# Kernel tuning notes

Measured on AMD Instinct MI355X. Metric: run time of the kernel, lower is better.

The kernel has to match this reference:

```python
import jax, jax.numpy as jnp
import numpy as np

DIM = 512
NUM_HEAD = 8
HEAD_DIM = DIM // NUM_HEAD
FFN = 4 * DIM


def setup_inputs() -> dict:
    key = jax.random.key(0)
    ks = jax.random.split(key, 16)
    s = DIM ** -0.5
    inp = {
        "x": jax.random.normal(ks[0], (4, 2048, DIM), jnp.float32),
        "wq": jax.random.normal(ks[1], (DIM, DIM), jnp.float32) * s,
        "bq": jnp.zeros((DIM,), jnp.float32),
        "wk": jax.random.normal(ks[2], (DIM, DIM), jnp.float32) * s,
        "bk": jnp.zeros((DIM,), jnp.float32),
        "wv": jax.random.normal(ks[3], (DIM, DIM), jnp.float32) * s,
        "bv": jnp.zeros((DIM,), jnp.float32),
        "wo": jax.random.normal(ks[4], (DIM, DIM), jnp.float32) * s,
        "bo": jnp.zeros((DIM,), jnp.float32),
        "w1": jax.random.normal(ks[5], (DIM, FFN), jnp.float32) * s,
        "b1": jnp.zeros((FFN,), jnp.float32),
        "w2": jax.random.normal(ks[6], (FFN, DIM), jnp.float32) * (FFN ** -0.5),
        "b2": jnp.zeros((DIM,), jnp.float32),
        "g1": jnp.ones((DIM,), jnp.float32),
        "be1": jnp.zeros((DIM,), jnp.float32),
        "g2": jnp.ones((DIM,), jnp.float32),
        "be2": jnp.zeros((DIM,), jnp.float32),
    }
    return inp


def layer_norm(x, g, b, eps=1e-5):
    mu = jnp.mean(x, axis=-1, keepdims=True)
    var = jnp.var(x, axis=-1, keepdims=True)
    return (x - mu) * jax.lax.rsqrt(var + eps) * g + b


def _forward(x, wq, bq, wk, bk, wv, bv, wo, bo, w1, b1, w2, b2, g1, be1, g2, be2):
    b, n, _ = x.shape
    scale = HEAD_DIM ** -0.5
    q = (x @ wq + bq).reshape(b, n, NUM_HEAD, HEAD_DIM).transpose(0, 2, 1, 3)
    k = (x @ wk + bk).reshape(b, n, NUM_HEAD, HEAD_DIM).transpose(0, 2, 1, 3)
    v = (x @ wv + bv).reshape(b, n, NUM_HEAD, HEAD_DIM).transpose(0, 2, 1, 3)
    scores = jnp.einsum('bhqd,bhkd->bhqk', q, k) * scale
    attn = jax.nn.softmax(scores, axis=-1)
    out = jnp.einsum('bhqk,bhkd->bhqd', attn, v)
    out = out.transpose(0, 2, 1, 3).reshape(b, n, DIM)
    out = out @ wo + bo
    x = layer_norm(out + x, g1, be1)
    h = jax.nn.gelu(x @ w1 + b1, approximate=False)
    ff = h @ w2 + b2
    x = layer_norm(ff + x, g2, be2)
    return x


def reference(x, wq, bq, wk, bk, wv, bv, wo, bo, w1, b1, w2, b2, g1, be1, g2, be2):
    return _forward(x, wq, bq, wk, bk, wv, bv, wo, bo, w1, b1, w2, b2, g1, be1, g2, be2)
```

## Files before the change

### kernel.cpp

```cpp
#include <hip/hip_runtime.h>
#include <math.h>

#define DIM 512
#define NHEAD 8
#define HD 64
#define FFN_DIM 2048
#define BATCH 4
#define SEQ 2048
#define MTOK (BATCH*SEQ)

typedef __attribute__((ext_vector_type(8))) short bf16x8;
typedef __attribute__((ext_vector_type(4))) float f32x4;

__device__ __forceinline__ unsigned short f2b(float f){
    unsigned int u = __float_as_uint(f);
    u += 0x7fffu + ((u >> 16) & 1u);
    return (unsigned short)(u >> 16);
}
__device__ __forceinline__ float b2f(unsigned short u){
    return __uint_as_float(((unsigned int)u) << 16);
}
__device__ __forceinline__ unsigned int pack_trunc(float f0, float f1){
    return __builtin_amdgcn_perm(__float_as_uint(f1), __float_as_uint(f0), 0x07060302u);
}
__device__ __forceinline__ void async_cp16(const unsigned short* g, unsigned short* l){
    __builtin_amdgcn_global_load_lds((const __attribute__((address_space(1))) unsigned int*)g,
                                     (__attribute__((address_space(3))) unsigned int*)l, 16, 0, 0);
}
__device__ __forceinline__ float gelu_fast(float x){
    float x3 = x*x*x;
    float y  = 2.302588f * (x + 0.044715f*x3);
    float t  = __builtin_amdgcn_exp2f(y);
    return x * t * __builtin_amdgcn_rcpf(t + 1.0f);
}

__device__ __forceinline__ void transp32(const float* __restrict__ in, unsigned short* __restrict__ out,
                                         int N, int K, int n0_rd, int n0_wr, int k0,
                                         unsigned short (&t)[32][33], int tid){
    int tx = tid & 31, ty = tid >> 5;
    #pragma unroll
    for (int u = 0; u < 4; u++)
        t[tx][ty + 8*u] = f2b(in[(size_t)(k0 + ty + 8*u)*N + n0_rd + tx]);
    __syncthreads();
    #pragma unroll
    for (int u = 0; u < 4; u++)
        out[(size_t)(n0_wr + ty + 8*u)*K + k0 + tx] = t[ty + 8*u][tx];
}

__global__ void prep_kernel(const float* __restrict__ x,
                            const float* __restrict__ wq, const float* __restrict__ wk,
                            const float* __restrict__ wv, const float* __restrict__ wo,
                            const float* __restrict__ w1, const float* __restrict__ w2,
                            const float* __restrict__ bq, const float* __restrict__ bk,
                            const float* __restrict__ bv,
                            unsigned short* __restrict__ xb, unsigned short* __restrict__ wqkvT,
                            unsigned short* __restrict__ woT, unsigned short* __restrict__ w1T,
                            unsigned short* __restrict__ w2T, float* __restrict__ bqkv)
{
    __shared__ unsigned short t[32][33];
    int bid = blockIdx.x, tid = threadIdx.x;
    if (bid < 4096) {
        int i = (bid*256 + tid)*4;
        float4 v = *(const float4*)(x + i);
        ushort4 o; o.x=f2b(v.x); o.y=f2b(v.y); o.z=f2b(v.z); o.w=f2b(v.w);
        *(ushort4*)(xb + i) = o;
    } else if (bid < 4864) {
        int r = bid - 4096;
        int n0 = (r % 48)*32, k0 = (r / 48)*32;
        const float* w = (n0 < 512) ? wq : (n0 < 1024) ? wk : wv;
        transp32(w, wqkvT, 512, 512, n0 & 511, n0, k0, t, tid);
    } else if (bid < 5120) {
        int r = bid - 4864;
        int n0 = (r % 16)*32, k0 = (r / 16)*32;
        transp32(wo, woT, 512, 512, n0, n0, k0, t, tid);
    } else if (bid < 6144) {
        int r = bid - 5120;
        int n0 = (r % 64)*32, k0 = (r / 64)*32;
        transp32(w1, w1T, 2048, 512, n0, n0, k0, t, tid);
    } else if (bid < 7168) {
        int r = bid - 6144;
        int n0 = (r % 16)*32, k0 = (r / 16)*32;
        transp32(w2, w2T, 512, 2048, n0, n0, k0, t, tid);
    } else {
        int i = (bid - 7168)*256 + tid;
        if (i < 1536)
            bqkv[i] = (i < 512) ? bq[i] : (i < 1024) ? bk[i-512] : bv[i-1024];
    }
}

template<int MODE, int SK>
__global__ __launch_bounds__(256, 4)
void gemm_bf16(const unsigned short* __restrict__ A, const unsigned short* __restrict__ Bt,
               const float* __restrict__ bias,
               unsigned short* __restrict__ Cb,
               unsigned short* __restrict__ qo, unsigned short* __restrict__ ko,
               unsigned short* __restrict__ vTo,
               int M, int N, int K)
{
    __shared__ unsigned short As[128*64];
    __shared__ unsigned short Bs[128*64];
    int tid  = threadIdx.x;
    int lane = tid & 63;
    int ln = lane & 15, qd = lane >> 4;
    int m0 = blockIdx.x * 128, n0 = blockIdx.y * 128;
    int wid = tid >> 6;
    int wm = (wid >> 1) * 64;
    int wn = (wid & 1) * 64;
    int kbeg = (SK > 1) ? (int)blockIdx.z * (K/SK) : 0;
    int kend = kbeg + K/SK;
    if (SK > 1 && MODE == 0) Cb += (size_t)blockIdx.z * M * N;

    f32x4 acc[4][4];
    #pragma unroll
    for (int i = 0; i < 4; i++)
        #pragma unroll
        for (int j = 0; j < 4; j++) acc[i][j] = (f32x4){0.f,0.f,0.f,0.f};

    for (int k0 = kbeg; k0 < kend; k0 += 64) {
        #pragma unroll
        for (int i = 0; i < 4; i++) {
            int cid = i*256 + tid;
            int row = cid >> 3, cs = cid & 7;
            int cg = cs ^ (row & 7);
            async_cp16(&A[(size_t)(m0+row)*K + k0 + cg*8], &As[(cid & ~63) * 8]);
        }
        #pragma unroll
        for (int i = 0; i < 4; i++) {
            int cid = i*256 + tid;
            int row = cid >> 3, cs = cid & 7;
            int cg = cs ^ (row & 7);
            async_cp16(&Bt[(size_t)(n0+row)*K + k0 + cg*8], &Bs[(cid & ~63) * 8]);
        }
        __syncthreads();
        #pragma unroll
        for (int kk = 0; kk < 64; kk += 32) {
            int c0 = kk >> 3;
            bf16x8 af[4], bf[4];
            #pragma unroll
            for (int t = 0; t < 4; t++)
                af[t] = *(bf16x8*)&As[(wm + t*16 + ln)*64 + ((c0 + qd) ^ (ln & 7))*8];
            #pragma unroll
            for (int t = 0; t < 4; t++)
                bf[t] = *(bf16x8*)&Bs[(wn + t*16 + ln)*64 + ((c0 + qd) ^ (ln & 7))*8];
            #pragma unroll
            for (int i = 0; i < 4; i++)
                #pragma unroll
                for (int j = 0; j < 4; j++)
                    acc[i][j] = __builtin_amdgcn_mfma_f32_16x16x32_bf16(af[i], bf[j], acc[i][j], 0,0,0);
        }
        __syncthreads();
    }

    const float QSCALE = 0.18033688011112042f;
    #pragma unroll
    for (int i = 0; i < 4; i++) {
        int mb = m0 + wm + i*16 + qd*4;
        #pragma unroll
        for (int j = 0; j < 4; j++) {
            int c = n0 + wn + j*16 + ln;
            float bv_ = (SK > 1 && blockIdx.z) ? 0.f : bias[c];
            float v[4];
            #pragma unroll
            for (int r = 0; r < 4; r++) v[r] = acc[i][j][r] + bv_;
            if (MODE == 0) {
                #pragma unroll
                for (int r = 0; r < 4; r++) Cb[(size_t)(mb+r)*N + c] = f2b(v[r]);
            } else if (MODE == 2) {
                #pragma unroll
                for (int r = 0; r < 4; r++)
                    Cb[(size_t)(mb+r)*N + c] = f2b(gelu_fast(v[r]));
            } else {
                int b = mb >> 11, t0 = mb & 2047;
                if (c < 512) {
                    int h = c >> 6, hd = c & 63;
                    #pragma unroll
                    for (int r = 0; r < 4; r++)
                        qo[(((size_t)(b*8 + h))*SEQ + t0 + r)*64 + hd] = f2b(v[r] * QSCALE);
                } else if (c < 1024) {
                    int cc = c - 512, h = cc >> 6, hd = cc & 63;
                    #pragma unroll
                    for (int r = 0; r < 4; r++)
                        ko[(((size_t)(b*8 + h))*SEQ + t0 + r)*64 + hd] = f2b(v[r]);
                } else {
                    int cc = c - 1024, h = cc >> 6, hd = cc & 63;
                    ushort4 pk;
                    pk.x = f2b(v[0]); pk.y = f2b(v[1]); pk.z = f2b(v[2]); pk.w = f2b(v[3]);
                    *(ushort4*)&vTo[(((size_t)(b*8 + h))*64 + hd)*SEQ + t0] = pk;
                }
            }
        }
    }
}

__global__ __launch_bounds__(256)
void attn_mfma(const unsigned short* __restrict__ Q, const unsigned short* __restrict__ K,
               const unsigned short* __restrict__ VT, unsigned short* __restrict__ O)
{
    __shared__ unsigned short lds[24576];
    unsigned short* Qs = lds + 8192;
    unsigned short* Ps = lds + 16384;
    int tid  = threadIdx.x;
    int wid  = tid >> 6, lane = tid & 63;
    int ln = lane & 15, qd = lane >> 4;
    int qb = blockIdx.x, bh = blockIdx.y;

    #pragma unroll
    for (int i = 0; i < 4; i++) {
        int cid = i*256 + tid;
        int row = cid >> 3, cs = cid & 7;
        int cg = cs ^ (row & 7);
        async_cp16(&Q[((size_t)bh*SEQ + qb*128 + row)*64 + cg*8], &Qs[(cid & ~63)*8]);
    }
    #pragma unroll
    for (int i = 0; i < 2; i++) {
        int cid = i*256 + tid;
        int row = cid >> 3, cs = cid & 7;
        int cg = cs ^ (row & 7);
        async_cp16(&K [((size_t)bh*SEQ + row)*64 + cg*8], &lds[(cid & ~63)*8]);
        async_cp16(&VT[((size_t)bh*64 + row)*SEQ + cg*8], &lds[4096 + (cid & ~63)*8]);
    }
    __syncthreads();

    bf16x8 qf[2][2];
    #pragma unroll
    for (int qs = 0; qs < 2; qs++)
        #pragma unroll
        for (int kk = 0; kk < 2; kk++)
            qf[qs][kk] = *(bf16x8*)&Qs[(wid*32 + qs*16 + ln)*64 + ((kk*4 + qd) ^ (ln & 7))*8];
    __syncthreads();

    f32x4 o[2][4];
    #pragma unroll
    for (int qs = 0; qs < 2; qs++)
        #pragma unroll
        for (int dt = 0; dt < 4; dt++) o[qs][dt] = (f32x4){0.f,0.f,0.f,0.f};
    float l_i[2] = {0.f, 0.f};

    for (int kt = 0; kt < 32; kt++) {
        int kof = (kt & 1) * 8192;
        int vof = 4096 + kof;
        if (kt < 31) {
            int nkof = 8192 - kof;
            #pragma unroll
            for (int i = 0; i < 2; i++) {
                int cid = i*256 + tid;
                int row = cid >> 3, cs = cid & 7;
                int cg = cs ^ (row & 7);
                async_cp16(&K [((size_t)bh*SEQ + (kt+1)*64 + row)*64 + cg*8], &lds[nkof + (cid & ~63)*8]);
                async_cp16(&VT[((size_t)bh*64 + row)*SEQ + (kt+1)*64 + cg*8], &lds[nkof + 4096 + (cid & ~63)*8]);
            }
        }

        f32x4 s[2][4];
        #pragma unroll
        for (int qs = 0; qs < 2; qs++)
            #pragma unroll
            for (int nt = 0; nt < 4; nt++) s[qs][nt] = (f32x4){0.f,0.f,0.f,0.f};
        #pragma unroll
        for (int kk = 0; kk < 2; kk++) {
            #pragma unroll
            for (int nt = 0; nt < 4; nt++) {
                bf16x8 kf = *(bf16x8*)&lds[kof + (nt*16 + ln)*64 + ((kk*4 + qd) ^ (ln & 7))*8];
                s[0][nt] = __builtin_amdgcn_mfma_f32_16x16x32_bf16(kf, qf[0][kk], s[0][nt], 0,0,0);
                s[1][nt] = __builtin_amdgcn_mfma_f32_16x16x32_bf16(kf, qf[1][kk], s[1][nt], 0,0,0);
            }
        }

        #pragma unroll
        for (int qs = 0; qs < 2; qs++) {
            #pragma unroll
            for (int nt = 0; nt < 4; nt++) {
                #pragma unroll
                for (int r = 0; r < 4; r++) {
                    float p = __builtin_amdgcn_exp2f(s[qs][nt][r]);
                    s[qs][nt][r] = p;
                    l_i[qs] += p;
                }
                uint2 pk;
                pk.x = pack_trunc(s[qs][nt][0], s[qs][nt][1]);
                pk.y = pack_trunc(s[qs][nt][2], s[qs][nt][3]);
                *(uint2*)&Ps[(wid*32 + qs*16 + ln)*64 + ((nt*2 + (qd>>1)) ^ (ln & 7))*8 + (qd&1)*4] = pk;
            }
        }

        #pragma unroll
        for (int kk = 0; kk < 2; kk++) {
            bf16x8 pf0 = *(bf16x8*)&Ps[(wid*32 + ln)*64      + ((kk*4 + qd) ^ (ln & 7))*8];
            bf16x8 pf1 = *(bf16x8*)&Ps[(wid*32 + 16 + ln)*64 + ((kk*4 + qd) ^ (ln & 7))*8];
            #pragma unroll
            for (int dt = 0; dt < 4; dt++) {
                bf16x8 vf = *(bf16x8*)&lds[vof + (dt*16 + ln)*64 + ((kk*4 + qd) ^ (ln & 7))*8];
                o[0][dt] = __builtin_amdgcn_mfma_f32_16x16x32_bf16(vf, pf0, o[0][dt], 0,0,0);
                o[1][dt] = __builtin_amdgcn_mfma_f32_16x16x32_bf16(vf, pf1, o[1][dt], 0,0,0);
            }
        }
        __syncthreads();
    }

    int b = bh >> 3, h = bh & 7;
    #pragma unroll
    for (int qs = 0; qs < 2; qs++) {
        float l = l_i[qs];
        l += __shfl_xor(l, 16);
        l += __shfl_xor(l, 32);
        float linv = 1.0f / l;
        int t = qb*128 + wid*32 + qs*16 + ln;
        #pragma unroll
        for (int dt = 0; dt < 4; dt++) {
            ushort4 pk;
            pk.x = f2b(o[qs][dt][0]*linv); pk.y = f2b(o[qs][dt][1]*linv);
            pk.z = f2b(o[qs][dt][2]*linv); pk.w = f2b(o[qs][dt][3]*linv);
            *(ushort4*)&O[((size_t)b*SEQ + t)*DIM + h*64 + dt*16 + qd*4] = pk;
        }
    }
}

__global__ void ln1_kernel(const unsigned short* __restrict__ m0b, const unsigned short* __restrict__ m1b,
                           const float* __restrict__ resp,
                           const float* __restrict__ g, const float* __restrict__ be,
                           unsigned short* __restrict__ outb)
{
    int row  = blockIdx.x*4 + (threadIdx.x >> 6);
    int lane = threadIdx.x & 63;
    size_t base = (size_t)row * DIM + lane*8;

    ushort4 a0 = *(const ushort4*)(m0b + base);
    ushort4 a1 = *(const ushort4*)(m0b + base + 4);
    ushort4 c0 = *(const ushort4*)(m1b + base);
    ushort4 c1 = *(const ushort4*)(m1b + base + 4);
    float4 r0 = *(const float4*)(resp + base);
    float4 r1 = *(const float4*)(resp + base + 4);
    float v[8] = { b2f(a0.x)+b2f(c0.x)+r0.x, b2f(a0.y)+b2f(c0.y)+r0.y,
                   b2f(a0.z)+b2f(c0.z)+r0.z, b2f(a0.w)+b2f(c0.w)+r0.w,
                   b2f(a1.x)+b2f(c1.x)+r1.x, b2f(a1.y)+b2f(c1.y)+r1.y,
                   b2f(a1.z)+b2f(c1.z)+r1.z, b2f(a1.w)+b2f(c1.w)+r1.w };
    float s = 0.f, s2 = 0.f;
    #pragma unroll
    for (int i = 0; i < 8; i++) { s += v[i]; s2 += v[i]*v[i]; }
    #pragma unroll
    for (int d = 32; d >= 1; d >>= 1) { s += __shfl_xor(s, d); s2 += __shfl_xor(s2, d); }
    float mean = s * (1.0f / DIM);
    float rstd = rsqrtf(s2 * (1.0f / DIM) - mean*mean + 1e-5f);

    float4 g0 = *(const float4*)(g + lane*8);
    float4 g1 = *(const float4*)(g + lane*8 + 4);
    float4 b0 = *(const float4*)(be + lane*8);
    float4 b1 = *(const float4*)(be + lane*8 + 4);
    float gg[8] = {g0.x,g0.y,g0.z,g0.w,g1.x,g1.y,g1.z,g1.w};
    float bb[8] = {b0.x,b0.y,b0.z,b0.w,b1.x,b1.y,b1.z,b1.w};
    float o[8];
    #pragma unroll
    for (int i = 0; i < 8; i++) o[i] = (v[i]-mean)*rstd*gg[i] + bb[i];
    ushort4 p0, p1;
    p0.x=f2b(o[0]); p0.y=f2b(o[1]); p0.z=f2b(o[2]); p0.w=f2b(o[3]);
    p1.x=f2b(o[4]); p1.y=f2b(o[5]); p1.z=f2b(o[6]); p1.w=f2b(o[7]);
    *(ushort4*)(outb + base)     = p0;
    *(ushort4*)(outb + base + 4) = p1;
}

__global__ void ln2_kernel(const unsigned short* __restrict__ m0b, const unsigned short* __restrict__ m1b,
                           const unsigned short* __restrict__ resb,
                           const float* __restrict__ g, const float* __restrict__ be,
                           float* __restrict__ outf)
{
    int row  = blockIdx.x*4 + (threadIdx.x >> 6);
    int lane = threadIdx.x & 63;
    size_t base = (size_t)row * DIM + lane*8;

    ushort4 a0 = *(const ushort4*)(m0b + base);
    ushort4 a1 = *(const ushort4*)(m0b + base + 4);
    ushort4 c0 = *(const ushort4*)(m1b + base);
    ushort4 c1 = *(const ushort4*)(m1b + base + 4);
    ushort4 rb0 = *(const ushort4*)(resb + base);
    ushort4 rb1 = *(const ushort4*)(resb + base + 4);
    float v[8] = { b2f(a0.x)+b2f(c0.x)+b2f(rb0.x), b2f(a0.y)+b2f(c0.y)+b2f(rb0.y),
                   b2f(a0.z)+b2f(c0.z)+b2f(rb0.z), b2f(a0.w)+b2f(c0.w)+b2f(rb0.w),
                   b2f(a1.x)+b2f(c1.x)+b2f(rb1.x), b2f(a1.y)+b2f(c1.y)+b2f(rb1.y),
                   b2f(a1.z)+b2f(c1.z)+b2f(rb1.z), b2f(a1.w)+b2f(c1.w)+b2f(rb1.w) };
    float s = 0.f, s2 = 0.f;
    #pragma unroll
    for (int i = 0; i < 8; i++) { s += v[i]; s2 += v[i]*v[i]; }
    #pragma unroll
    for (int d = 32; d >= 1; d >>= 1) { s += __shfl_xor(s, d); s2 += __shfl_xor(s2, d); }
    float mean = s * (1.0f / DIM);
    float rstd = rsqrtf(s2 * (1.0f / DIM) - mean*mean + 1e-5f);

    float4 g0 = *(const float4*)(g + lane*8);
    float4 g1 = *(const float4*)(g + lane*8 + 4);
    float4 b0 = *(const float4*)(be + lane*8);
    float4 b1 = *(const float4*)(be + lane*8 + 4);
    float gg[8] = {g0.x,g0.y,g0.z,g0.w,g1.x,g1.y,g1.z,g1.w};
    float bb[8] = {b0.x,b0.y,b0.z,b0.w,b1.x,b1.y,b1.z,b1.w};
    float o[8];
    #pragma unroll
    for (int i = 0; i < 8; i++) o[i] = (v[i] - mean)*rstd*gg[i] + bb[i];
    *(float4*)(outf + base)     = (float4){o[0],o[1],o[2],o[3]};
    *(float4*)(outf + base + 4) = (float4){o[4],o[5],o[6],o[7]};
}

extern "C" void kernel_launch(void* const* d_in, const int* in_sizes, int n_in,
                              void* d_out, int out_size, void* d_ws, size_t ws_size,
                              hipStream_t stream) {
    const float* x   = (const float*)d_in[0];
    const float* wq  = (const float*)d_in[1];
    const float* bq  = (const float*)d_in[2];
    const float* wk  = (const float*)d_in[3];
    const float* bk  = (const float*)d_in[4];
    const float* wv  = (const float*)d_in[5];
    const float* bv  = (const float*)d_in[6];
    const float* wo  = (const float*)d_in[7];
    const float* bo  = (const float*)d_in[8];
    const float* w1  = (const float*)d_in[9];
    const float* b1  = (const float*)d_in[10];
    const float* w2  = (const float*)d_in[11];
    const float* b2  = (const float*)d_in[12];
    const float* g1  = (const float*)d_in[13];
    const float* be1 = (const float*)d_in[14];
    const float* g2  = (const float*)d_in[15];
    const float* be2 = (const float*)d_in[16];
    float* out = (float*)d_out;

    char* w = (char*)d_ws;
    size_t off = 0;
    auto alloc = [&](size_t bytes){ void* p = w + off; off += (bytes + 255) & ~(size_t)255; return p; };
    unsigned short* xb     = (unsigned short*)alloc((size_t)MTOK*DIM*2);
    unsigned short* wqkvT  = (unsigned short*)alloc((size_t)1536*512*2);
    unsigned short* woT    = (unsigned short*)alloc((size_t)512*512*2);
    unsigned short* w1T    = (unsigned short*)alloc((size_t)2048*512*2);
    unsigned short* w2T    = (unsigned short*)alloc((size_t)512*2048*2);
    float*          bqkv   = (float*)alloc(1536*4);
    unsigned short* qb_    = (unsigned short*)alloc((size_t)32*SEQ*64*2);
    unsigned short* kb_    = (unsigned short*)alloc((size_t)32*SEQ*64*2);
    unsigned short* vT_    = (unsigned short*)alloc((size_t)32*64*SEQ*2);
    unsigned short* attno  = (unsigned short*)alloc((size_t)MTOK*DIM*2);
    unsigned short* x1b    = (unsigned short*)alloc((size_t)MTOK*DIM*2);
    unsigned short* h_     = (unsigned short*)alloc((size_t)MTOK*FFN_DIM*2);
    unsigned short* ffb    = (unsigned short*)alloc((size_t)2*MTOK*DIM*2);

    prep_kernel<<<7174, 256, 0, stream>>>(x, wq, wk, wv, wo, w1, w2, bq, bk, bv,
                                          xb, wqkvT, woT, w1T, w2T, bqkv);

    gemm_bf16<1,1><<<dim3(64,12), 256, 0, stream>>>(xb, wqkvT, bqkv, nullptr,
                                                    qb_, kb_, vT_, MTOK, 1536, DIM);
    attn_mfma<<<dim3(16,32), 256, 0, stream>>>(qb_, kb_, vT_, attno);
    gemm_bf16<0,2><<<dim3(64,4,2), 256, 0, stream>>>(attno, woT, bo, ffb,
                                                     nullptr, nullptr, nullptr, MTOK, DIM, DIM);
    ln1_kernel<<<MTOK/4, 256, 0, stream>>>(ffb, ffb + (size_t)MTOK*DIM, x, g1, be1, x1b);
    gemm_bf16<2,1><<<dim3(64,16), 256, 0, stream>>>(x1b, w1T, b1, h_,
                                                    nullptr, nullptr, nullptr, MTOK, FFN_DIM, DIM);
    gemm_bf16<0,2><<<dim3(64,4,2), 256, 0, stream>>>(h_, w2T, b2, ffb,
                                                     nullptr, nullptr, nullptr, MTOK, DIM, FFN_DIM);
    ln2_kernel<<<MTOK/4, 256, 0, stream>>>(ffb, ffb + (size_t)MTOK*DIM, x1b, g2, be2, out);
}
```

Measured before the change: 256.5 us.

## Triple-buffer attention K/V, keep P in registers, remap block indices

The attention kernel moves from double to triple buffering of K/V tiles. Explicit vmcnt waits and raw barriers replace the per-iteration __syncthreads, so loads run two tiles ahead. The softmax probabilities stay in registers and feed a 16x16x16 MFMA directly, which removes the P round-trip through LDS. A 1D grid with a swizzled block-to-(head, query block) mapping is meant to improve K/V cache reuse. The risks are a wrong vmcnt count under hand synchronization and the smaller MFMA shape issuing more instructions.

```diff
diff --git a/kernel.cpp b/kernel.cpp
--- a/kernel.cpp
+++ b/kernel.cpp
@@ -10,6 +10,7 @@
 #define MTOK (BATCH*SEQ)
 
 typedef __attribute__((ext_vector_type(8))) short bf16x8;
+typedef __attribute__((ext_vector_type(4))) short bf16x4;
 typedef __attribute__((ext_vector_type(4))) float f32x4;
 
 __device__ __forceinline__ unsigned short f2b(float f){
@@ -26,6 +27,10 @@
 __device__ __forceinline__ void async_cp16(const unsigned short* g, unsigned short* l){
     __builtin_amdgcn_global_load_lds((const __attribute__((address_space(1))) unsigned int*)g,
                                      (__attribute__((address_space(3))) unsigned int*)l, 16, 0, 0);
+}
+__device__ __forceinline__ f32x4 mfma16(bf16x4 a, bf16x4 b, f32x4 c){
+    asm("v_mfma_f32_16x16x16_bf16 %0, %1, %2, %0" : "+v"(c) : "v"(a), "v"(b));
+    return c;
 }
 __device__ __forceinline__ float gelu_fast(float x){
     float x3 = x*x*x;
@@ -197,37 +202,41 @@
                const unsigned short* __restrict__ VT, unsigned short* __restrict__ O)
 {
     __shared__ unsigned short lds[24576];
-    unsigned short* Qs = lds + 8192;
-    unsigned short* Ps = lds + 16384;
     int tid  = threadIdx.x;
     int wid  = tid >> 6, lane = tid & 63;
     int ln = lane & 15, qd = lane >> 4;
-    int qb = blockIdx.x, bh = blockIdx.y;
+    int bx = blockIdx.x;
+    int qb = (bx >> 3) & 15;
+    int bh = (bx & 7) + 8 * (bx >> 7);
 
     #pragma unroll
     for (int i = 0; i < 4; i++) {
         int cid = i*256 + tid;
-        int row = cid >> 3, cs = cid & 7;
-        int cg = cs ^ (row & 7);
-        async_cp16(&Q[((size_t)bh*SEQ + qb*128 + row)*64 + cg*8], &Qs[(cid & ~63)*8]);
-    }
-    #pragma unroll
-    for (int i = 0; i < 2; i++) {
-        int cid = i*256 + tid;
-        int row = cid >> 3, cs = cid & 7;
-        int cg = cs ^ (row & 7);
-        async_cp16(&K [((size_t)bh*SEQ + row)*64 + cg*8], &lds[(cid & ~63)*8]);
-        async_cp16(&VT[((size_t)bh*64 + row)*SEQ + cg*8], &lds[4096 + (cid & ~63)*8]);
-    }
-    __syncthreads();
+        int row = cid >> 3, cs = cid & 7, cg = cs ^ (row & 7);
+        async_cp16(&Q[((size_t)bh*SEQ + qb*128 + row)*64 + cg*8], &lds[16384 + (cid & ~63)*8]);
+    }
+    #pragma unroll
+    for (int t = 0; t < 2; t++) {
+        #pragma unroll
+        for (int i = 0; i < 2; i++) {
+            int cid = i*256 + tid;
+            int row = cid >> 3, cs = cid & 7, cg = cs ^ (row & 7);
+            async_cp16(&K [((size_t)bh*SEQ + t*64 + row)*64 + cg*8], &lds[t*8192 + (cid & ~63)*8]);
+            async_cp16(&VT[((size_t)bh*64 + row)*SEQ + t*64 + cg*8], &lds[t*8192 + 4096 + (cid & ~63)*8]);
+        }
+    }
+    asm volatile("s_waitcnt vmcnt(8)" ::: "memory");
+    __builtin_amdgcn_s_barrier();
+    __builtin_amdgcn_sched_barrier(0);
 
     bf16x8 qf[2][2];
     #pragma unroll
     for (int qs = 0; qs < 2; qs++)
         #pragma unroll
         for (int kk = 0; kk < 2; kk++)
-            qf[qs][kk] = *(bf16x8*)&Qs[(wid*32 + qs*16 + ln)*64 + ((kk*4 + qd) ^ (ln & 7))*8];
-    __syncthreads();
+            qf[qs][kk] = *(bf16x8*)&lds[16384 + (wid*32 + qs*16 + ln)*64 + ((kk*4 + qd) ^ (ln & 7))*8];
+    asm volatile("s_waitcnt lgkmcnt(0)" ::: "memory");
+    __builtin_amdgcn_sched_barrier(0);
 
     f32x4 o[2][4];
     #pragma unroll
@@ -237,19 +246,22 @@
     float l_i[2] = {0.f, 0.f};
 
     for (int kt = 0; kt < 32; kt++) {
-        int kof = (kt & 1) * 8192;
-        int vof = 4096 + kof;
-        if (kt < 31) {
-            int nkof = 8192 - kof;
+        if (kt < 31) { asm volatile("s_waitcnt vmcnt(4)" ::: "memory"); }
+        else         { asm volatile("s_waitcnt vmcnt(0)" ::: "memory"); }
+        __builtin_amdgcn_s_barrier();
+        __builtin_amdgcn_sched_barrier(0);
+        if (kt < 30) {
+            int nb = ((kt+2) % 3) * 8192;
             #pragma unroll
             for (int i = 0; i < 2; i++) {
                 int cid = i*256 + tid;
-                int row = cid >> 3, cs = cid & 7;
-                int cg = cs ^ (row & 7);
-                async_cp16(&K [((size_t)bh*SEQ + (kt+1)*64 + row)*64 + cg*8], &lds[nkof + (cid & ~63)*8]);
-                async_cp16(&VT[((size_t)bh*64 + row)*SEQ + (kt+1)*64 + cg*8], &lds[nkof + 4096 + (cid & ~63)*8]);
+                int row = cid >> 3, cs = cid & 7, cg = cs ^ (row & 7);
+                async_cp16(&K [((size_t)bh*SEQ + (kt+2)*64 + row)*64 + cg*8], &lds[nb + (cid & ~63)*8]);
+                async_cp16(&VT[((size_t)bh*64 + row)*SEQ + (kt+2)*64 + cg*8], &lds[nb + 4096 + (cid & ~63)*8]);
             }
         }
+        int kof = (kt % 3) * 8192;
+        int vof = kof + 4096;
 
         f32x4 s[2][4];
         #pragma unroll
@@ -266,36 +278,36 @@
             }
         }
 
+        bf16x4 pf[2][4];
         #pragma unroll
         for (int qs = 0; qs < 2; qs++) {
             #pragma unroll
             for (int nt = 0; nt < 4; nt++) {
-                #pragma unroll
-                for (int r = 0; r < 4; r++) {
-                    float p = __builtin_amdgcn_exp2f(s[qs][nt][r]);
-                    s[qs][nt][r] = p;
-                    l_i[qs] += p;
-                }
+                float p0 = __builtin_amdgcn_exp2f(s[qs][nt][0]);
+                float p1 = __builtin_amdgcn_exp2f(s[qs][nt][1]);
+                float p2 = __builtin_amdgcn_exp2f(s[qs][nt][2]);
+                float p3 = __builtin_amdgcn_exp2f(s[qs][nt][3]);
+                l_i[qs] += (p0 + p1) + (p2 + p3);
                 uint2 pk;
-                pk.x = pack_trunc(s[qs][nt][0], s[qs][nt][1]);
-                pk.y = pack_trunc(s[qs][nt][2], s[qs][nt][3]);
-                *(uint2*)&Ps[(wid*32 + qs*16 + ln)*64 + ((nt*2 + (qd>>1)) ^ (ln & 7))*8 + (qd&1)*4] = pk;
+                pk.x = pack_trunc(p0, p1);
+                pk.y = pack_trunc(p2, p3);
+                pf[qs][nt] = __builtin_bit_cast(bf16x4, pk);
             }
         }
 
         #pragma unroll
-        for (int kk = 0; kk < 2; kk++) {
-            bf16x8 pf0 = *(bf16x8*)&Ps[(wid*32 + ln)*64      + ((kk*4 + qd) ^ (ln & 7))*8];
-            bf16x8 pf1 = *(bf16x8*)&Ps[(wid*32 + 16 + ln)*64 + ((kk*4 + qd) ^ (ln & 7))*8];
+        for (int nt = 0; nt < 4; nt++) {
             #pragma unroll
             for (int dt = 0; dt < 4; dt++) {
-                bf16x8 vf = *(bf16x8*)&lds[vof + (dt*16 + ln)*64 + ((kk*4 + qd) ^ (ln & 7))*8];
-                o[0][dt] = __builtin_amdgcn_mfma_f32_16x16x32_bf16(vf, pf0, o[0][dt], 0,0,0);
-                o[1][dt] = __builtin_amdgcn_mfma_f32_16x16x32_bf16(vf, pf1, o[1][dt], 0,0,0);
+                bf16x4 vf = *(bf16x4*)&lds[vof + (dt*16 + ln)*64
+                                           + ((nt*2 + (qd>>1)) ^ (ln & 7))*8 + (qd & 1)*4];
+                o[0][dt] = mfma16(vf, pf[0][nt], o[0][dt]);
+                o[1][dt] = mfma16(vf, pf[1][nt], o[1][dt]);
             }
         }
-        __syncthreads();
-    }
+    }
+    asm volatile("s_nop 7");
+    asm volatile("s_nop 7");
 
     int b = bh >> 3, h = bh & 7;
     #pragma unroll
@@ -442,7 +454,7 @@
 
     gemm_bf16<1,1><<<dim3(64,12), 256, 0, stream>>>(xb, wqkvT, bqkv, nullptr,
                                                     qb_, kb_, vT_, MTOK, 1536, DIM);
-    attn_mfma<<<dim3(16,32), 256, 0, stream>>>(qb_, kb_, vT_, attno);
+    attn_mfma<<<512, 256, 0, stream>>>(qb_, kb_, vT_, attno);
     gemm_bf16<0,2><<<dim3(64,4,2), 256, 0, stream>>>(attno, woT, bo, ffb,
                                                      nullptr, nullptr, nullptr, MTOK, DIM, DIM);
     ln1_kernel<<<MTOK/4, 256, 0, stream>>>(ffb, ffb + (size_t)MTOK*DIM, x, g1, be1, x1b);
```

New measurement: 252.8 us. No clear change (-1.4%).
